# Optimization experiments

Hardware: AMD Instinct MI355X
Metric: run time of the kernel (lower is better)

Reference implementation:

```python
import jax, jax.numpy as jnp
import numpy as np


def setup_inputs() -> dict:
    key = jax.random.key(0)
    k1, k2 = jax.random.split(key)
    B, D, H, W = 16, 256, 32, 32
    K = 2048
    z = jax.random.normal(k1, (B, D, H, W), dtype=jnp.float32)
    # EmbeddingEMA init: uniform(-1/K, 1/K); plain randn scaled works as a stand-in param
    codebook = jax.random.uniform(k2, (K, D), dtype=jnp.float32,
                                  minval=-1.0 / K, maxval=1.0 / K)
    return {"z": z, "codebook": codebook}


def reference(z, codebook):
    # z: (B, D, H, W) -> (B, H, W, D) -> (n, D)   [normalize == 'none' path]
    B, D, H, W = z.shape
    z_flat = jnp.transpose(z, (0, 2, 3, 1)).reshape(-1, D)          # (n, D)
    z_norm = z_flat
    codebook_norm = codebook                                         # (K, D)

    # squared L2 distance: ||z||^2 + ||c||^2 - 2 z c^T   -> (n, K)
    distance = (jnp.sum(z_norm * z_norm, axis=1, keepdims=True)
                + jnp.sum(codebook_norm * codebook_norm, axis=1)
                - 2.0 * jnp.matmul(z_norm, codebook_norm.T))

    vq_indices = jnp.argmin(distance, axis=1)                        # (n,)
    z_q = codebook_norm[vq_indices]                                  # gather (n, D)

    # straight-through estimator (standard VQ forward output)
    z_q_st = z_norm + jax.lax.stop_gradient(z_q - z_norm)
    out = z_q_st.reshape(B, H, W, D).transpose(0, 3, 1, 2)           # (B, D, H, W)
    return out
```

## Files before the change

kernel.cpp:

```cpp
#include <hip/hip_runtime.h>


#define D_  256
#define K_  2048
#define HW_ 1024
#define MT  32
#define NT  256
#define KT  32
#define CST 258

__device__ __forceinline__ float pw8(const float r[8]) {
    float t01 = __fadd_rn(r[0], r[1]);
    float t23 = __fadd_rn(r[2], r[3]);
    float L   = __fadd_rn(t01, t23);
    float t45 = __fadd_rn(r[4], r[5]);
    float t67 = __fadd_rn(r[6], r[7]);
    float R   = __fadd_rn(t45, t67);
    return __fadd_rn(L, R);
}

__global__ __launch_bounds__(256) void bn_k(const float* __restrict__ cb,
                                            float* __restrict__ Bn) {
    int row = blockIdx.x * 256 + threadIdx.x;
    const float4* p = reinterpret_cast<const float4*>(cb + (size_t)row * D_);
    float rA[8], rB[8];
    #pragma unroll
    for (int j = 0; j < 8; ++j) { rA[j] = 0.f; rB[j] = 0.f; }
    #pragma unroll
    for (int q = 0; q < 64; ++q) {
        float4 v = p[q];
        float pv[4] = {__fmul_rn(v.x, v.x), __fmul_rn(v.y, v.y),
                       __fmul_rn(v.z, v.z), __fmul_rn(v.w, v.w)};
        if (q < 32) {
            #pragma unroll
            for (int l = 0; l < 4; ++l) {
                int j = (4 * q + l) & 7;
                rA[j] = __fadd_rn(rA[j], pv[l]);
            }
        } else {
            #pragma unroll
            for (int l = 0; l < 4; ++l) {
                int j = (4 * q + l) & 7;
                rB[j] = __fadd_rn(rB[j], pv[l]);
            }
        }
    }
    Bn[row] = __fadd_rn(pw8(rA), pw8(rB));
}

__global__ __launch_bounds__(256) void an_k(const float* __restrict__ z,
                                            float* __restrict__ An) {
    __shared__ float ls[KT][256];
    int b      = blockIdx.x >> 2;
    int hwbase = (blockIdx.x & 3) << 8;
    const float* zb = z + (size_t)b * (D_ * HW_) + hwbase;
    int tid = threadIdx.x;
    float rA[8], rB[8];
    #pragma unroll
    for (int j = 0; j < 8; ++j) { rA[j] = 0.f; rB[j] = 0.f; }
    for (int kc = 0; kc < 8; ++kc) {
        __syncthreads();
        #pragma unroll
        for (int it = 0; it < 8; ++it) {
            int u  = (it << 8) + tid;
            int dd = u >> 6;
            int m4 = u & 63;
            float4 v = *reinterpret_cast<const float4*>(
                zb + (size_t)(kc * KT + dd) * HW_ + (m4 << 2));
            *reinterpret_cast<float4*>(&ls[dd][m4 << 2]) = v;
        }
        __syncthreads();
        if (kc < 4) {
            #pragma unroll
            for (int dd = 0; dd < 32; ++dd) {
                float v = ls[dd][tid];
                rA[dd & 7] = __fadd_rn(rA[dd & 7], __fmul_rn(v, v));
            }
        } else {
            #pragma unroll
            for (int dd = 0; dd < 32; ++dd) {
                float v = ls[dd][tid];
                rB[dd & 7] = __fadd_rn(rB[dd & 7], __fmul_rn(v, v));
            }
        }
    }
    An[(size_t)b * HW_ + hwbase + tid] = __fadd_rn(pw8(rA), pw8(rB));
}

__global__ __launch_bounds__(256, 2) void vq_k(const float* __restrict__ z,
                                               const float* __restrict__ cb,
                                               const float* __restrict__ An,
                                               const float* __restrict__ Bn,
                                               float* __restrict__ out) {
    __shared__ float zs[KT][MT];
    __shared__ float cs[KT * CST];
    __shared__ float rs[MT * 33];
    __shared__ int   ri[MT * 33];
    __shared__ int   idxs[MT];

    const int tid = threadIdx.x;
    const int tn  = tid & 31;
    const int tm  = tid >> 5;
    const int blk = blockIdx.x;
    const int b      = blk >> 5;
    const int hwbase = (blk & 31) << 5;
    const float* zbase = z + (size_t)b * (D_ * HW_) + hwbase;

    float an[4];
    #pragma unroll
    for (int i = 0; i < 4; ++i)
        an[i] = An[(size_t)b * HW_ + hwbase + (tm << 2) + i];

    float bs[4] = {1e30f, 1e30f, 1e30f, 1e30f};
    int   bi[4] = {0, 0, 0, 0};

    for (int nc = 0; nc < K_ / NT; ++nc) {
        float acc[4][8];
        #pragma unroll
        for (int i = 0; i < 4; ++i)
            #pragma unroll
            for (int j = 0; j < 8; ++j) acc[i][j] = 0.f;

        for (int kc = 0; kc < D_ / KT; ++kc) {
            __syncthreads();
            {
                int dd = tid >> 3;
                int m4 = tid & 7;
                float4 v = *reinterpret_cast<const float4*>(
                    zbase + (size_t)(kc * KT + dd) * HW_ + (m4 << 2));
                *reinterpret_cast<float4*>(&zs[dd][m4 << 2]) = v;
            }
            {
                const float* cbase = cb + (size_t)(nc * NT) * D_ + kc * KT;
                #pragma unroll
                for (int it = 0; it < 8; ++it) {
                    int u  = (it << 8) + tid;
                    int nn = u >> 3;
                    int d4 = u & 7;
                    float4 v = *reinterpret_cast<const float4*>(
                        cbase + (size_t)nn * D_ + (d4 << 2));
                    int db = d4 << 2;
                    cs[(db + 0) * CST + nn] = v.x;
                    cs[(db + 1) * CST + nn] = v.y;
                    cs[(db + 2) * CST + nn] = v.z;
                    cs[(db + 3) * CST + nn] = v.w;
                }
            }
            __syncthreads();
            #pragma unroll
            for (int d = 0; d < KT; ++d) {
                float4 a = *reinterpret_cast<const float4*>(&zs[d][tm << 2]);
                const float* crow = &cs[d * CST + (tn << 1)];
                float2 b0 = *reinterpret_cast<const float2*>(crow);
                float2 b1 = *reinterpret_cast<const float2*>(crow + 64);
                float2 b2 = *reinterpret_cast<const float2*>(crow + 128);
                float2 b3 = *reinterpret_cast<const float2*>(crow + 192);
                float av[4] = {a.x, a.y, a.z, a.w};
                float bv[8] = {b0.x, b0.y, b1.x, b1.y, b2.x, b2.y, b3.x, b3.y};
                #pragma unroll
                for (int i = 0; i < 4; ++i)
                    #pragma unroll
                    for (int j = 0; j < 8; ++j)
                        acc[i][j] = fmaf(av[i], bv[j], acc[i][j]);
            }
        }
        #pragma unroll
        for (int j = 0; j < 8; ++j) {
            int nl = (j & 1) + (tn << 1) + ((j >> 1) << 6);
            int ng = nc * NT + nl;
            float bn = Bn[ng];
            #pragma unroll
            for (int i = 0; i < 4; ++i) {
                float sc = __fsub_rn(__fadd_rn(an[i], bn),
                                     __fmul_rn(2.0f, acc[i][j]));
                if (sc < bs[i]) { bs[i] = sc; bi[i] = ng; }
            }
        }
    }

    #pragma unroll
    for (int i = 0; i < 4; ++i) {
        int m = (tm << 2) + i;
        rs[m * 33 + tn] = bs[i];
        ri[m * 33 + tn] = bi[i];
    }
    __syncthreads();
    if (tid < MT) {
        int   m    = tid;
        float best = rs[m * 33];
        int   bidx = ri[m * 33];
        for (int t = 1; t < 32; ++t) {
            float s  = rs[m * 33 + t];
            int   ix = ri[m * 33 + t];
            if (s < best || (s == best && ix < bidx)) { best = s; bidx = ix; }
        }
        idxs[m] = bidx;
    }
    __syncthreads();

    float* obase = out + (size_t)b * (D_ * HW_) + hwbase;
    #pragma unroll
    for (int it = 0; it < 8; ++it) {
        int u  = (it << 8) + tid;
        int dd = u >> 3;
        int m4 = u & 7;
        int i0 = idxs[(m4 << 2) + 0];
        int i1 = idxs[(m4 << 2) + 1];
        int i2 = idxs[(m4 << 2) + 2];
        int i3 = idxs[(m4 << 2) + 3];
        float4 o;
        o.x = cb[(size_t)i0 * D_ + dd];
        o.y = cb[(size_t)i1 * D_ + dd];
        o.z = cb[(size_t)i2 * D_ + dd];
        o.w = cb[(size_t)i3 * D_ + dd];
        *reinterpret_cast<float4*>(obase + (size_t)dd * HW_ + (m4 << 2)) = o;
    }
}

extern "C" void kernel_launch(void* const* d_in, const int* in_sizes, int n_in,
                              void* d_out, int out_size, void* d_ws, size_t ws_size,
                              hipStream_t stream) {
    const float* z  = (const float*)d_in[0];
    const float* cb = (const float*)d_in[1];
    float* An = (float*)d_ws;
    float* Bn = (float*)d_ws + 16384;
    float* out = (float*)d_out;

    bn_k<<<dim3(K_ / 256), dim3(256), 0, stream>>>(cb, Bn);
    an_k<<<dim3(64), dim3(256), 0, stream>>>(z, An);
    vq_k<<<dim3(16384 / MT), dim3(256), 0, stream>>>(z, cb, An, Bn, out);
}
```

Baseline: 342.6 us.

## Split codebook search across blocks with 8x8 register tiles and a finalize kernel

Result: slower. 423.0 us (+23.4%).

```diff
diff --git a/kernel.cpp b/kernel.cpp
--- a/kernel.cpp
+++ b/kernel.cpp
@@ -1,13 +1,16 @@
 #include <hip/hip_runtime.h>
 
 
-#define D_  256
-#define K_  2048
-#define HW_ 1024
-#define MT  32
-#define NT  256
-#define KT  32
-#define CST 258
+#define D_    256
+#define K_    2048
+#define HW_   1024
+#define MT    64
+#define NT    256
+#define KT    32
+#define SPLIT 4
+#define KS    (K_ / SPLIT)
+#define CST   258
+#define NPIX  16384
 
 __device__ __forceinline__ float pw8(const float r[8]) {
     float t01 = __fadd_rn(r[0], r[1]);
@@ -33,16 +36,10 @@
                        __fmul_rn(v.z, v.z), __fmul_rn(v.w, v.w)};
         if (q < 32) {
             #pragma unroll
-            for (int l = 0; l < 4; ++l) {
-                int j = (4 * q + l) & 7;
-                rA[j] = __fadd_rn(rA[j], pv[l]);
-            }
+            for (int l = 0; l < 4; ++l) rA[(4 * q + l) & 7] = __fadd_rn(rA[(4 * q + l) & 7], pv[l]);
         } else {
             #pragma unroll
-            for (int l = 0; l < 4; ++l) {
-                int j = (4 * q + l) & 7;
-                rB[j] = __fadd_rn(rB[j], pv[l]);
-            }
+            for (int l = 0; l < 4; ++l) rB[(4 * q + l) & 7] = __fadd_rn(rB[(4 * q + l) & 7], pv[l]);
         }
     }
     Bn[row] = __fadd_rn(pw8(rA), pw8(rB));
@@ -87,51 +84,62 @@
     An[(size_t)b * HW_ + hwbase + tid] = __fadd_rn(pw8(rA), pw8(rB));
 }
 
-__global__ __launch_bounds__(256, 2) void vq_k(const float* __restrict__ z,
+__global__ __launch_bounds__(256, 3) void vq_k(const float* __restrict__ z,
                                                const float* __restrict__ cb,
                                                const float* __restrict__ An,
                                                const float* __restrict__ Bn,
-                                               float* __restrict__ out) {
-    __shared__ float zs[KT][MT];
-    __shared__ float cs[KT * CST];
-    __shared__ float rs[MT * 33];
-    __shared__ int   ri[MT * 33];
-    __shared__ int   idxs[MT];
+                                               float* __restrict__ pscore,
+                                               int* __restrict__ pidx) {
+    __shared__ float smem[KT * MT + KT * CST];
+    float* zs = smem;
+    float* cs = smem + KT * MT;
+    float* rs = smem;
+    int*   ri = (int*)(smem + MT * 33);
+    int*   idxs = (int*)(smem + 2 * MT * 33);
 
     const int tid = threadIdx.x;
-    const int tn  = tid & 31;
-    const int tm  = tid >> 5;
+    const int wv  = tid >> 6;
+    const int tn  = (tid & 7) | (wv << 3);
+    const int tm  = (tid >> 3) & 7;
     const int blk = blockIdx.x;
-    const int b      = blk >> 5;
-    const int hwbase = (blk & 31) << 5;
+    const int p   = blk >> 2;
+    const int s   = blk & 3;
+    const int b      = p >> 4;
+    const int hwbase = (p & 15) << 6;
     const float* zbase = z + (size_t)b * (D_ * HW_) + hwbase;
-
-    float an[4];
-    #pragma unroll
-    for (int i = 0; i < 4; ++i)
-        an[i] = An[(size_t)b * HW_ + hwbase + (tm << 2) + i];
-
-    float bs[4] = {1e30f, 1e30f, 1e30f, 1e30f};
-    int   bi[4] = {0, 0, 0, 0};
-
-    for (int nc = 0; nc < K_ / NT; ++nc) {
-        float acc[4][8];
-        #pragma unroll
-        for (int i = 0; i < 4; ++i)
+    const float* cbS   = cb + (size_t)s * KS * D_;
+
+    float an[8];
+    #pragma unroll
+    for (int i = 0; i < 8; ++i)
+        an[i] = An[(size_t)b * HW_ + hwbase + (tm << 3) + i];
+
+    float bs[8]; int bi[8];
+    #pragma unroll
+    for (int i = 0; i < 8; ++i) { bs[i] = 1e30f; bi[i] = 0; }
+
+    for (int nc = 0; nc < KS / NT; ++nc) {
+        float acc[8][8];
+        #pragma unroll
+        for (int i = 0; i < 8; ++i)
             #pragma unroll
             for (int j = 0; j < 8; ++j) acc[i][j] = 0.f;
 
         for (int kc = 0; kc < D_ / KT; ++kc) {
             __syncthreads();
             {
-                int dd = tid >> 3;
-                int m4 = tid & 7;
-                float4 v = *reinterpret_cast<const float4*>(
-                    zbase + (size_t)(kc * KT + dd) * HW_ + (m4 << 2));
-                *reinterpret_cast<float4*>(&zs[dd][m4 << 2]) = v;
+                #pragma unroll
+                for (int it = 0; it < 2; ++it) {
+                    int u  = (it << 8) + tid;
+                    int dd = u >> 4;
+                    int m4 = u & 15;
+                    float4 v = *reinterpret_cast<const float4*>(
+                        zbase + (size_t)(kc * KT + dd) * HW_ + (m4 << 2));
+                    *reinterpret_cast<float4*>(&zs[dd * MT + (m4 << 2)]) = v;
+                }
             }
             {
-                const float* cbase = cb + (size_t)(nc * NT) * D_ + kc * KT;
+                const float* cbase = cbS + (size_t)(nc * NT) * D_ + kc * KT;
                 #pragma unroll
                 for (int it = 0; it < 8; ++it) {
                     int u  = (it << 8) + tid;
@@ -149,16 +157,16 @@
             __syncthreads();
             #pragma unroll
             for (int d = 0; d < KT; ++d) {
-                float4 a = *reinterpret_cast<const float4*>(&zs[d][tm << 2]);
-                const float* crow = &cs[d * CST + (tn << 1)];
-                float2 b0 = *reinterpret_cast<const float2*>(crow);
-                float2 b1 = *reinterpret_cast<const float2*>(crow + 64);
-                float2 b2 = *reinterpret_cast<const float2*>(crow + 128);
-                float2 b3 = *reinterpret_cast<const float2*>(crow + 192);
-                float av[4] = {a.x, a.y, a.z, a.w};
-                float bv[8] = {b0.x, b0.y, b1.x, b1.y, b2.x, b2.y, b3.x, b3.y};
+                const float* zr = &zs[d * MT + (tm << 3)];
+                float4 a0 = *reinterpret_cast<const float4*>(zr);
+                float4 a1 = *reinterpret_cast<const float4*>(zr + 4);
+                const float* crow = &cs[d * CST + (tn << 3)];
+                float4 b0 = *reinterpret_cast<const float4*>(crow);
+                float4 b1 = *reinterpret_cast<const float4*>(crow + 4);
+                float av[8] = {a0.x, a0.y, a0.z, a0.w, a1.x, a1.y, a1.z, a1.w};
+                float bv[8] = {b0.x, b0.y, b0.z, b0.w, b1.x, b1.y, b1.z, b1.w};
                 #pragma unroll
-                for (int i = 0; i < 4; ++i)
+                for (int i = 0; i < 8; ++i)
                     #pragma unroll
                     for (int j = 0; j < 8; ++j)
                         acc[i][j] = fmaf(av[i], bv[j], acc[i][j]);
@@ -166,11 +174,11 @@
         }
         #pragma unroll
         for (int j = 0; j < 8; ++j) {
-            int nl = (j & 1) + (tn << 1) + ((j >> 1) << 6);
-            int ng = nc * NT + nl;
+            int nl = (tn << 3) + j;
+            int ng = s * KS + nc * NT + nl;
             float bn = Bn[ng];
             #pragma unroll
-            for (int i = 0; i < 4; ++i) {
+            for (int i = 0; i < 8; ++i) {
                 float sc = __fsub_rn(__fadd_rn(an[i], bn),
                                      __fmul_rn(2.0f, acc[i][j]));
                 if (sc < bs[i]) { bs[i] = sc; bi[i] = ng; }
@@ -178,9 +186,10 @@
         }
     }
 
-    #pragma unroll
-    for (int i = 0; i < 4; ++i) {
-        int m = (tm << 2) + i;
+    __syncthreads();
+    #pragma unroll
+    for (int i = 0; i < 8; ++i) {
+        int m = (tm << 3) + i;
         rs[m * 33 + tn] = bs[i];
         ri[m * 33 + tn] = bi[i];
     }
@@ -190,20 +199,44 @@
         float best = rs[m * 33];
         int   bidx = ri[m * 33];
         for (int t = 1; t < 32; ++t) {
-            float s  = rs[m * 33 + t];
+            float sv = rs[m * 33 + t];
             int   ix = ri[m * 33 + t];
-            if (s < best || (s == best && ix < bidx)) { best = s; bidx = ix; }
-        }
-        idxs[m] = bidx;
+            if (sv < best || (sv == best && ix < bidx)) { best = sv; bidx = ix; }
+        }
+        int g = b * HW_ + hwbase + m;
+        pscore[s * NPIX + g] = best;
+        pidx[s * NPIX + g]   = bidx;
+    }
+}
+
+__global__ __launch_bounds__(256) void fin_k(const float* __restrict__ cb,
+                                             const float* __restrict__ pscore,
+                                             const int* __restrict__ pidx,
+                                             float* __restrict__ out) {
+    __shared__ int idxs[MT];
+    int tid = threadIdx.x;
+    int p   = blockIdx.x;
+    int b      = p >> 4;
+    int hwbase = (p & 15) << 6;
+    if (tid < MT) {
+        int g = b * HW_ + hwbase + tid;
+        float best = pscore[g];
+        int   bidx = pidx[g];
+        #pragma unroll
+        for (int s = 1; s < SPLIT; ++s) {
+            float sv = pscore[s * NPIX + g];
+            int   ix = pidx[s * NPIX + g];
+            if (sv < best || (sv == best && ix < bidx)) { best = sv; bidx = ix; }
+        }
+        idxs[tid] = bidx;
     }
     __syncthreads();
-
     float* obase = out + (size_t)b * (D_ * HW_) + hwbase;
     #pragma unroll
-    for (int it = 0; it < 8; ++it) {
+    for (int it = 0; it < 16; ++it) {
         int u  = (it << 8) + tid;
-        int dd = u >> 3;
-        int m4 = u & 7;
+        int dd = u >> 4;
+        int m4 = u & 15;
         int i0 = idxs[(m4 << 2) + 0];
         int i1 = idxs[(m4 << 2) + 1];
         int i2 = idxs[(m4 << 2) + 2];
@@ -222,11 +255,14 @@
                               hipStream_t stream) {
     const float* z  = (const float*)d_in[0];
     const float* cb = (const float*)d_in[1];
-    float* An = (float*)d_ws;
-    float* Bn = (float*)d_ws + 16384;
-    float* out = (float*)d_out;
+    float* An     = (float*)d_ws;
+    float* Bn     = An + NPIX;
+    float* pscore = Bn + K_;
+    int*   pidx   = (int*)(pscore + SPLIT * NPIX);
+    float* out    = (float*)d_out;
 
     bn_k<<<dim3(K_ / 256), dim3(256), 0, stream>>>(cb, Bn);
     an_k<<<dim3(64), dim3(256), 0, stream>>>(z, An);
-    vq_k<<<dim3(16384 / MT), dim3(256), 0, stream>>>(z, cb, An, Bn, out);
-}
+    vq_k<<<dim3(256 * SPLIT), dim3(256), 0, stream>>>(z, cb, An, Bn, pscore, pidx);
+    fin_k<<<dim3(256), dim3(256), 0, stream>>>(cb, pscore, pidx, out);
+}
```
